# Kernel tuning notes

Measured on AMD Instinct MI355X. Metric: run time of the kernel, lower is better.

The kernel has to match this reference:

```python
import jax, jax.numpy as jnp
import numpy as np

NUM_CODES = 1024
CODE_DIM = 256
EMA_DECAY = 0.99
EPSILON = 1e-05
SOFTMAX_TEMP = 0.1


def setup_inputs() -> dict:
    key = jax.random.key(0)
    k1, k2, k3 = jax.random.split(key, 3)
    z = jax.random.normal(k1, (32, 1024, CODE_DIM), dtype=jnp.float32)
    embed = jax.random.normal(k2, (NUM_CODES, CODE_DIM), dtype=jnp.float32) * 0.1
    cluster_size = jnp.ones((NUM_CODES,), dtype=jnp.float32)
    embed_avg = jax.random.normal(k3, (NUM_CODES, CODE_DIM), dtype=jnp.float32) * 0.1
    return {"z": z, "embed": embed, "cluster_size": cluster_size, "embed_avg": embed_avg}


def reference(z, embed, cluster_size, embed_avg):
    orig_shape = z.shape
    flat_z = z.reshape(-1, CODE_DIM)                      # [N, D]
    N = flat_z.shape[0]

    # squared euclidean distances: [N, K]
    dist = (jnp.sum(flat_z * flat_z, axis=1, keepdims=True)
            - 2.0 * jnp.einsum('nd,kd->nk', flat_z, embed)
            + jnp.sum(embed * embed, axis=1)[None, :])

    codes = jnp.argmin(dist, axis=1)                      # [N]
    z_q = embed[codes]                                    # [N, D]
    soft_assign = jax.nn.softmax(-dist / SOFTMAX_TEMP, axis=-1)

    # EMA updates (training branch), functional: return new buffers
    counts = jax.ops.segment_sum(jnp.ones((N,), dtype=flat_z.dtype), codes,
                                 num_segments=NUM_CODES)            # encodings.sum(0)
    embed_sum = jax.ops.segment_sum(flat_z, codes, num_segments=NUM_CODES)  # [K, D]
    new_cluster_size = EMA_DECAY * cluster_size + (1.0 - EMA_DECAY) * counts
    new_embed_avg = EMA_DECAY * embed_avg + (1.0 - EMA_DECAY) * embed_sum
    n = jnp.sum(new_cluster_size)
    cs_norm = (new_cluster_size + EPSILON) / (n + NUM_CODES * EPSILON) * n
    new_embed = new_embed_avg / cs_norm[:, None]

    commitment_loss = jnp.mean((flat_z - jax.lax.stop_gradient(z_q)) ** 2)

    # straight-through estimator
    z_q_st = (flat_z + jax.lax.stop_gradient(z_q - flat_z)).reshape(orig_shape)
    codes_out = codes.reshape(orig_shape[:-1])

    avg_probs = counts / N
    log_p = jnp.log(avg_probs + 1e-10)
    code_entropy = -jnp.sum(avg_probs * log_p)
    perplexity = jnp.exp(code_entropy)

    soft_assign_out = soft_assign.reshape(*orig_shape[:-1], NUM_CODES)
    return (z_q_st, codes_out, commitment_loss, perplexity, code_entropy,
            soft_assign_out, new_embed, new_cluster_size, new_embed_avg)
```

## Files before the change

### kernel.cpp

```cpp
#include <hip/hip_runtime.h>
#include <math.h>

#define N_ROWS 32768
#define DIM 256
#define K_CODES 1024

#define WS_LOSS   0
#define WS_NSUM   1024
#define WS_ZZ     2048
#define WS_EE     34816
#define WS_COUNTS 35840
#define WS_ESUM   36864
#define WS_TOTAL  (36864 + K_CODES * DIM)

#define OFF_ZQ    0ull
#define OFF_CODES 8388608ull
#define OFF_LOSS  8421376ull
#define OFF_PERP  8421377ull
#define OFF_ENT   8421378ull
#define OFF_SOFT  8421379ull
#define OFF_NEMB  41975811ull
#define OFF_NCS   42237955ull
#define OFF_NEA   42238979ull


typedef __attribute__((ext_vector_type(8))) short bf16x8;
typedef __attribute__((ext_vector_type(4))) float f32x4;

__device__ __forceinline__ ushort f2bf(float x) {
    union { float f; unsigned u; } a; a.f = x;
    unsigned r = a.u + 0x7fffu + ((a.u >> 16) & 1u);
    return (ushort)(r >> 16);
}
__device__ __forceinline__ float bf2f(ushort h) {
    union { unsigned u; float f; } a; a.u = ((unsigned)h) << 16;
    return a.f;
}

__global__ __launch_bounds__(256) void k0_zero(float* ws) {
    int i = blockIdx.x * 256 + threadIdx.x;
    if (i < WS_TOTAL) ws[i] = 0.0f;
}

__global__ __launch_bounds__(256) void k1_norms(const float* __restrict__ z,
                                                const float* __restrict__ embed,
                                                float* __restrict__ ws,
                                                float* out) {
    ushort* zhi = (ushort*)(out + OFF_ZQ);
    ushort* zlo = zhi + (size_t)N_ROWS * DIM;
    ushort* ehi = (ushort*)(out + OFF_NEMB);
    ushort* elo = ehi + (size_t)K_CODES * DIM;

    int wave = threadIdx.x >> 6;
    int lane = threadIdx.x & 63;
    int row = blockIdx.x * 4 + wave;
    const float* src = (row < N_ROWS) ? (z + (size_t)row * DIM)
                                      : (embed + (size_t)(row - N_ROWS) * DIM);
    float4 v = *(const float4*)(src + lane * 4);
    float s = v.x * v.x + v.y * v.y + v.z * v.z + v.w * v.w;

    ushort h0 = f2bf(v.x), h1 = f2bf(v.y), h2 = f2bf(v.z), h3 = f2bf(v.w);
    ushort l0 = f2bf(v.x - bf2f(h0)), l1 = f2bf(v.y - bf2f(h1));
    ushort l2 = f2bf(v.z - bf2f(h2)), l3 = f2bf(v.w - bf2f(h3));
    unsigned hA = (unsigned)h0 | ((unsigned)h1 << 16);
    unsigned hB = (unsigned)h2 | ((unsigned)h3 << 16);
    unsigned lA = (unsigned)l0 | ((unsigned)l1 << 16);
    unsigned lB = (unsigned)l2 | ((unsigned)l3 << 16);

    if (row < N_ROWS) {
        size_t o = (size_t)row * DIM + lane * 4;
        ((uint2*)(zhi + o))[0] = make_uint2(hA, hB);
        ((uint2*)(zlo + o))[0] = make_uint2(lA, lB);
    } else {
        size_t o = (size_t)(row - N_ROWS) * DIM + lane * 4;
        unsigned* ph = (unsigned*)(ehi + o);
        unsigned* pl = (unsigned*)(elo + o);
        ph[0] = hA; ph[1] = hB;
        pl[0] = lA; pl[1] = lB;
    }

    #pragma unroll
    for (int off = 32; off; off >>= 1) s += __shfl_down(s, off, 64);
    if (lane == 0) {
        if (row < N_ROWS) ws[WS_ZZ + row] = s;
        else              ws[WS_EE + (row - N_ROWS)] = s;
    }
}

__global__ __launch_bounds__(256, 3) void k2_mfma(const float* __restrict__ ws,
                                                  float* out) {
    const ushort* zhi = (const ushort*)(out + OFF_ZQ);
    const ushort* zlo = zhi + (size_t)N_ROWS * DIM;
    const ushort* ehi = (const ushort*)(out + OFF_NEMB);
    const ushort* elo = ehi + (size_t)K_CODES * DIM;

    int tid  = threadIdx.x;
    int lane = tid & 63;
    int wid  = tid >> 6;
    int wr   = wid >> 1, wc = wid & 1;
    int rowBase = blockIdx.y * 64 + wr * 32;
    int colBase = blockIdx.x * 256 + wc * 128;
    int l15 = lane & 15, lg = lane >> 4;
    int kof = lg * 8;

    f32x4 acc[2][8];
    #pragma unroll
    for (int fi = 0; fi < 2; ++fi)
        #pragma unroll
        for (int fj = 0; fj < 8; ++fj)
            acc[fi][fj] = (f32x4){0.f, 0.f, 0.f, 0.f};

    for (int kk = 0; kk < DIM; kk += 32) {
        bf16x8 ah[2], al[2];
        #pragma unroll
        for (int fi = 0; fi < 2; ++fi) {
            size_t ao = (size_t)(rowBase + fi * 16 + l15) * DIM + kk + kof;
            ah[fi] = *(const bf16x8*)(zhi + ao);
            al[fi] = *(const bf16x8*)(zlo + ao);
        }
        #pragma unroll
        for (int fj = 0; fj < 8; ++fj) {
            size_t bo = (size_t)(colBase + fj * 16 + l15) * DIM + kk + kof;
            union { unsigned u[4]; bf16x8 v; } bh, bl;
            const unsigned* ph = (const unsigned*)(ehi + bo);
            const unsigned* pl = (const unsigned*)(elo + bo);
            bh.u[0] = ph[0]; bh.u[1] = ph[1]; bh.u[2] = ph[2]; bh.u[3] = ph[3];
            bl.u[0] = pl[0]; bl.u[1] = pl[1]; bl.u[2] = pl[2]; bl.u[3] = pl[3];
            #pragma unroll
            for (int fi = 0; fi < 2; ++fi) {
                acc[fi][fj] = __builtin_amdgcn_mfma_f32_16x16x32_bf16(ah[fi], bh.v, acc[fi][fj], 0, 0, 0);
                acc[fi][fj] = __builtin_amdgcn_mfma_f32_16x16x32_bf16(ah[fi], bl.v, acc[fi][fj], 0, 0, 0);
                acc[fi][fj] = __builtin_amdgcn_mfma_f32_16x16x32_bf16(al[fi], bh.v, acc[fi][fj], 0, 0, 0);
            }
        }
    }

    #pragma unroll
    for (int fi = 0; fi < 2; ++fi) {
        #pragma unroll
        for (int q = 0; q < 4; ++q) {
            int n = rowBase + fi * 16 + lg * 4 + q;
            float zzn = ws[WS_ZZ + n];
            float* orow = out + OFF_SOFT + (size_t)n * K_CODES;
            #pragma unroll
            for (int fj = 0; fj < 8; ++fj) {
                int k = colBase + fj * 16 + l15;
                orow[k] = (zzn - 2.0f * acc[fi][fj][q]) + ws[WS_EE + k];
            }
        }
    }
}

__device__ inline void blockMinIdx(float& v, int& idx, float* smv, int* smi) {
    int lane = threadIdx.x & 63, wave = threadIdx.x >> 6;
    #pragma unroll
    for (int off = 32; off; off >>= 1) {
        float ov = __shfl_down(v, off, 64);
        int   oi = __shfl_down(idx, off, 64);
        if (ov < v || (ov == v && oi < idx)) { v = ov; idx = oi; }
    }
    if (lane == 0) { smv[wave] = v; smi[wave] = idx; }
    __syncthreads();
    v = smv[0]; idx = smi[0];
    #pragma unroll
    for (int w = 1; w < 4; ++w) {
        float ov = smv[w]; int oi = smi[w];
        if (ov < v || (ov == v && oi < idx)) { v = ov; idx = oi; }
    }
    __syncthreads();
}

__device__ inline float blockSum(float v, float* sm) {
    int lane = threadIdx.x & 63, wave = threadIdx.x >> 6;
    #pragma unroll
    for (int off = 32; off; off >>= 1) v += __shfl_down(v, off, 64);
    if (lane == 0) sm[wave] = v;
    __syncthreads();
    float r = sm[0] + sm[1] + sm[2] + sm[3];
    __syncthreads();
    return r;
}

__global__ __launch_bounds__(256) void k3_softmax(const float* __restrict__ z,
                                                  const float* __restrict__ embed,
                                                  float* __restrict__ ws,
                                                  float* __restrict__ out) {
    __shared__ float smv[4];
    __shared__ int   smi[4];
    __shared__ float sms[4];
    __shared__ double sdd[4];
    __shared__ int cand[8];
    __shared__ int ncand;

    int n = blockIdx.x;
    int tid = threadIdx.x;
    float* dptr = out + OFF_SOFT + (size_t)n * K_CODES;

    float d[4];
    float lmin = 3.4e38f; int lidx = 0;
    #pragma unroll
    for (int j = 0; j < 4; ++j) {
        int k = tid + 256 * j;
        d[j] = dptr[k];
        if (d[j] < lmin) { lmin = d[j]; lidx = k; }
    }
    float bmin = lmin; int code = lidx;
    blockMinIdx(bmin, code, smv, smi);

    if (tid == 0) ncand = 0;
    __syncthreads();
    #pragma unroll
    for (int j = 0; j < 4; ++j) {
        if (d[j] <= bmin + 1e-3f) {
            int slot = atomicAdd(&ncand, 1);
            if (slot < 8) cand[slot] = tid + 256 * j;
        }
    }
    __syncthreads();
    int nc = ncand;
    float zv = z[(size_t)n * DIM + tid];
    if (nc > 1) {
        int lim = nc < 8 ? nc : 8;
        float zzn = ws[WS_ZZ + n];
        float bestd = 0.f; int bestk = -1;
        for (int c = 0; c < lim; ++c) {
            int kc = cand[c];
            double part = (double)zv * (double)embed[(size_t)kc * DIM + tid];
            int lane = tid & 63, wave = tid >> 6;
            #pragma unroll
            for (int off = 32; off; off >>= 1) part += __shfl_down(part, off, 64);
            if (lane == 0) sdd[wave] = part;
            __syncthreads();
            double dot = sdd[0] + sdd[1] + sdd[2] + sdd[3];
            __syncthreads();
            float d32 = (zzn - 2.0f * (float)dot) + ws[WS_EE + kc];
            if (bestk < 0 || d32 < bestd || (d32 == bestd && kc < bestk)) { bestd = d32; bestk = kc; }
        }
        code = bestk;
    }

    float p[4]; float s = 0.f;
    #pragma unroll
    for (int j = 0; j < 4; ++j) { p[j] = __expf((bmin - d[j]) * 10.0f); s += p[j]; }
    float tot = blockSum(s, sms);
    float inv = 1.0f / tot;
    #pragma unroll
    for (int j = 0; j < 4; ++j) dptr[tid + 256 * j] = p[j] * inv;

    float qv = embed[(size_t)code * DIM + tid];
    out[OFF_ZQ + (size_t)n * DIM + tid] = qv;
    float diff = zv - qv;
    float lsum = blockSum(diff * diff, sms);
    atomicAdd(&ws[WS_ESUM + (size_t)code * DIM + tid], zv);
    if (tid == 0) {
        atomicAdd(&ws[WS_LOSS + (n & 1023)], lsum);
        atomicAdd(&ws[WS_COUNTS + code], 1.0f);
        out[OFF_CODES + n] = (float)code;
    }
}

__global__ __launch_bounds__(1024) void k4a_stats(const float* __restrict__ cluster_size,
                                                  float* __restrict__ ws,
                                                  float* __restrict__ out) {
    __shared__ float sm[16];
    int k = threadIdx.x;
    int lane = k & 63, wave = k >> 6;
    float cnt = ws[WS_COUNTS + k];
    float ncs = 0.99f * cluster_size[k] + 0.01f * cnt;
    out[OFF_NCS + k] = ncs;

    float v = ncs;
    #pragma unroll
    for (int off = 32; off; off >>= 1) v += __shfl_down(v, off, 64);
    if (lane == 0) sm[wave] = v;
    __syncthreads();
    if (k == 0) {
        float t = 0.f;
        for (int w = 0; w < 16; ++w) t += sm[w];
        ws[WS_NSUM] = t;
    }
    __syncthreads();

    float avg = cnt / (float)N_ROWS;
    v = -avg * logf(avg + 1e-10f);
    #pragma unroll
    for (int off = 32; off; off >>= 1) v += __shfl_down(v, off, 64);
    if (lane == 0) sm[wave] = v;
    __syncthreads();
    if (k == 0) {
        float ent = 0.f;
        for (int w = 0; w < 16; ++w) ent += sm[w];
        out[OFF_ENT]  = ent;
        out[OFF_PERP] = expf(ent);
    }
    __syncthreads();

    v = ws[WS_LOSS + k];
    #pragma unroll
    for (int off = 32; off; off >>= 1) v += __shfl_down(v, off, 64);
    if (lane == 0) sm[wave] = v;
    __syncthreads();
    if (k == 0) {
        float t = 0.f;
        for (int w = 0; w < 16; ++w) t += sm[w];
        out[OFF_LOSS] = t / 8388608.0f;
    }
}

__global__ __launch_bounds__(256) void k4b_embed(const float* __restrict__ embed_avg,
                                                 const float* __restrict__ ws,
                                                 float* __restrict__ out) {
    int k = blockIdx.x, d = threadIdx.x;
    float es  = ws[WS_ESUM + (size_t)k * DIM + d];
    float nea = 0.99f * embed_avg[(size_t)k * DIM + d] + 0.01f * es;
    out[OFF_NEA + (size_t)k * DIM + d] = nea;
    float ncs  = out[OFF_NCS + k];
    float nsum = ws[WS_NSUM];
    float csn  = (ncs + 1e-5f) / (nsum + K_CODES * 1e-5f) * nsum;
    out[OFF_NEMB + (size_t)k * DIM + d] = nea / csn;
}

extern "C" void kernel_launch(void* const* d_in, const int* in_sizes, int n_in,
                              void* d_out, int out_size, void* d_ws, size_t ws_size,
                              hipStream_t stream) {
    const float* z            = (const float*)d_in[0];
    const float* embed        = (const float*)d_in[1];
    const float* cluster_size = (const float*)d_in[2];
    const float* embed_avg    = (const float*)d_in[3];
    float* out = (float*)d_out;
    float* ws  = (float*)d_ws;

    k0_zero<<<(WS_TOTAL + 255) / 256, 256, 0, stream>>>(ws);
    k1_norms<<<(N_ROWS + K_CODES) / 4, 256, 0, stream>>>(z, embed, ws, out);
    k2_mfma<<<dim3(K_CODES / 256, N_ROWS / 64), 256, 0, stream>>>(ws, out);
    k3_softmax<<<N_ROWS, 256, 0, stream>>>(z, embed, ws, out);
    k4a_stats<<<1, 1024, 0, stream>>>(cluster_size, ws, out);
    k4b_embed<<<K_CODES, 256, 0, stream>>>(embed_avg, ws, out);
}
```

Measured before the change: 430.8 us.

## Pack bf16 hi/lo operands in MFMA fragment order for contiguous wave loads

The norms kernel now writes the split bf16 hi/lo copies of z and embed in a tiled layout matching the 16x16x32 MFMA fragment order, 512 elements per 16-row by 32-k block. The GEMM kernel can then load each fragment as one contiguous 16-byte vector per lane, so a wave reads 1 KB contiguously instead of 16-byte pieces strided by row. The embed packing moves to a 16-byte-aligned offset, which also allows the B loads to be vectorised rather than split into four 4-byte loads. The scatter writes in the norms kernel become less contiguous in exchange.

```diff
diff --git a/kernel.cpp b/kernel.cpp
--- a/kernel.cpp
+++ b/kernel.cpp
@@ -23,6 +23,10 @@
 #define OFF_NCS   42237955ull
 #define OFF_NEA   42238979ull
 
+#define OFF_EPACK 41975812ull
+#define PLANE_Z   8388608ull
+#define PLANE_E   262144ull
+
 
 typedef __attribute__((ext_vector_type(8))) short bf16x8;
 typedef __attribute__((ext_vector_type(4))) float f32x4;
@@ -47,9 +51,9 @@
                                                 float* __restrict__ ws,
                                                 float* out) {
     ushort* zhi = (ushort*)(out + OFF_ZQ);
-    ushort* zlo = zhi + (size_t)N_ROWS * DIM;
-    ushort* ehi = (ushort*)(out + OFF_NEMB);
-    ushort* elo = ehi + (size_t)K_CODES * DIM;
+    ushort* zlo = zhi + PLANE_Z;
+    ushort* ehi = (ushort*)(out + OFF_EPACK);
+    ushort* elo = ehi + PLANE_E;
 
     int wave = threadIdx.x >> 6;
     int lane = threadIdx.x & 63;
@@ -67,16 +71,19 @@
     unsigned lA = (unsigned)l0 | ((unsigned)l1 << 16);
     unsigned lB = (unsigned)l2 | ((unsigned)l3 << 16);
 
+    int r = (row < N_ROWS) ? row : (row - N_ROWS);
+    int kb = lane >> 3;
+    int lg = (lane >> 1) & 3;
+    int j0 = (lane & 1) * 4;
+    size_t idx = ((size_t)(r >> 4) * 8 + kb) * 512
+               + (size_t)(lg * 16 + (r & 15)) * 8 + j0;
+
     if (row < N_ROWS) {
-        size_t o = (size_t)row * DIM + lane * 4;
-        ((uint2*)(zhi + o))[0] = make_uint2(hA, hB);
-        ((uint2*)(zlo + o))[0] = make_uint2(lA, lB);
+        *(uint2*)(zhi + idx) = make_uint2(hA, hB);
+        *(uint2*)(zlo + idx) = make_uint2(lA, lB);
     } else {
-        size_t o = (size_t)(row - N_ROWS) * DIM + lane * 4;
-        unsigned* ph = (unsigned*)(ehi + o);
-        unsigned* pl = (unsigned*)(elo + o);
-        ph[0] = hA; ph[1] = hB;
-        pl[0] = lA; pl[1] = lB;
+        *(uint2*)(ehi + idx) = make_uint2(hA, hB);
+        *(uint2*)(elo + idx) = make_uint2(lA, lB);
     }
 
     #pragma unroll
@@ -90,9 +97,7 @@
 __global__ __launch_bounds__(256, 3) void k2_mfma(const float* __restrict__ ws,
                                                   float* out) {
     const ushort* zhi = (const ushort*)(out + OFF_ZQ);
-    const ushort* zlo = zhi + (size_t)N_ROWS * DIM;
-    const ushort* ehi = (const ushort*)(out + OFF_NEMB);
-    const ushort* elo = ehi + (size_t)K_CODES * DIM;
+    const ushort* ehi = (const ushort*)(out + OFF_EPACK);
 
     int tid  = threadIdx.x;
     int lane = tid & 63;
@@ -101,7 +106,6 @@
     int rowBase = blockIdx.y * 64 + wr * 32;
     int colBase = blockIdx.x * 256 + wc * 128;
     int l15 = lane & 15, lg = lane >> 4;
-    int kof = lg * 8;
 
     f32x4 acc[2][8];
     #pragma unroll
@@ -110,27 +114,27 @@
         for (int fj = 0; fj < 8; ++fj)
             acc[fi][fj] = (f32x4){0.f, 0.f, 0.f, 0.f};
 
-    for (int kk = 0; kk < DIM; kk += 32) {
+    int rowBlk = rowBase >> 4;
+    int colBlk = colBase >> 4;
+
+    for (int kb = 0; kb < 8; ++kb) {
         bf16x8 ah[2], al[2];
         #pragma unroll
         for (int fi = 0; fi < 2; ++fi) {
-            size_t ao = (size_t)(rowBase + fi * 16 + l15) * DIM + kk + kof;
-            ah[fi] = *(const bf16x8*)(zhi + ao);
-            al[fi] = *(const bf16x8*)(zlo + ao);
+            const ushort* pa = zhi + ((size_t)(rowBlk + fi) * 8 + kb) * 512 + lane * 8;
+            ah[fi] = *(const bf16x8*)pa;
+            al[fi] = *(const bf16x8*)(pa + PLANE_Z);
         }
         #pragma unroll
         for (int fj = 0; fj < 8; ++fj) {
-            size_t bo = (size_t)(colBase + fj * 16 + l15) * DIM + kk + kof;
-            union { unsigned u[4]; bf16x8 v; } bh, bl;
-            const unsigned* ph = (const unsigned*)(ehi + bo);
-            const unsigned* pl = (const unsigned*)(elo + bo);
-            bh.u[0] = ph[0]; bh.u[1] = ph[1]; bh.u[2] = ph[2]; bh.u[3] = ph[3];
-            bl.u[0] = pl[0]; bl.u[1] = pl[1]; bl.u[2] = pl[2]; bl.u[3] = pl[3];
+            const ushort* pb = ehi + ((size_t)(colBlk + fj) * 8 + kb) * 512 + lane * 8;
+            bf16x8 bh = *(const bf16x8*)pb;
+            bf16x8 bl = *(const bf16x8*)(pb + PLANE_E);
             #pragma unroll
             for (int fi = 0; fi < 2; ++fi) {
-                acc[fi][fj] = __builtin_amdgcn_mfma_f32_16x16x32_bf16(ah[fi], bh.v, acc[fi][fj], 0, 0, 0);
-                acc[fi][fj] = __builtin_amdgcn_mfma_f32_16x16x32_bf16(ah[fi], bl.v, acc[fi][fj], 0, 0, 0);
-                acc[fi][fj] = __builtin_amdgcn_mfma_f32_16x16x32_bf16(al[fi], bh.v, acc[fi][fj], 0, 0, 0);
+                acc[fi][fj] = __builtin_amdgcn_mfma_f32_16x16x32_bf16(ah[fi], bh, acc[fi][fj], 0, 0, 0);
+                acc[fi][fj] = __builtin_amdgcn_mfma_f32_16x16x32_bf16(ah[fi], bl, acc[fi][fj], 0, 0, 0);
+                acc[fi][fj] = __builtin_amdgcn_mfma_f32_16x16x32_bf16(al[fi], bh, acc[fi][fj], 0, 0, 0);
             }
         }
     }
```

New measurement: 369.4 us. -14.3%, faster.
